# Optimization experiments

Hardware: AMD Instinct MI355X
Metric: run time of the kernel (lower is better)

The kernel has to match this reference:

```python
import jax, jax.numpy as jnp
import numpy as np

Q_HEADS, KV_HEADS, DIMS, IN_DIMS = 16, 4, 1024, 1024
HEAD_D = DIMS // Q_HEADS            # 64
GROUPS = Q_HEADS // KV_HEADS        # 4
ROPE_BASE = 10000.0


def nd_rope(x, coords):
    """N-D rotary embedding.
    x: [..., s, d]; coords: broadcastable [..., s, a] (float).
    Head dim d is split into a contiguous chunks of d//a; within each chunk
    consecutive pairs (2i, 2i+1) are rotated by angle coord_axis * base^(-2i/(d//a)).
    """
    a = coords.shape[-1]
    d = x.shape[-1]
    dpa = d // a                                  # dims per coordinate axis (even)
    inv_freq = ROPE_BASE ** (-jnp.arange(dpa // 2, dtype=jnp.float32) * (2.0 / dpa))
    angles = coords[..., :, None] * inv_freq      # [..., s, a, dpa//2]
    angles = angles.reshape(angles.shape[:-2] + (d // 2,))
    cos, sin = jnp.cos(angles), jnp.sin(angles)
    xp = x.reshape(x.shape[:-1] + (d // 2, 2))
    x1, x2 = xp[..., 0], xp[..., 1]
    return jnp.stack([x1 * cos - x2 * sin, x1 * sin + x2 * cos], axis=-1).reshape(x.shape)


def setup_inputs() -> dict:
    key = jax.random.key(0)
    k1, k2, k3, k4, k5, k6, k7, k8 = jax.random.split(key, 8)
    B, SQ, SKV, A = 4, 2048, 2048, 2
    q = jax.random.normal(k1, (B, SQ, IN_DIMS), dtype=jnp.float32)
    kv = jax.random.normal(k2, (B, SKV, IN_DIMS), dtype=jnp.float32)
    q_coords = jax.random.randint(k3, (B, SQ, A), 0, 2048, dtype=jnp.int32)
    kv_coords = jax.random.randint(k4, (B, SKV, A), 0, 2048, dtype=jnp.int32)
    s_in = 1.0 / np.sqrt(IN_DIMS)
    Wq = jax.random.normal(k5, (IN_DIMS, Q_HEADS, HEAD_D), dtype=jnp.float32) * s_in
    Wk = jax.random.normal(k6, (IN_DIMS, KV_HEADS, HEAD_D), dtype=jnp.float32) * s_in
    Wv = jax.random.normal(k7, (IN_DIMS, KV_HEADS, HEAD_D), dtype=jnp.float32) * s_in
    Wo = jax.random.normal(k8, (KV_HEADS * HEAD_D, IN_DIMS), dtype=jnp.float32) * (1.0 / np.sqrt(KV_HEADS * HEAD_D))
    return {"q": q, "q_coords": q_coords, "kv": kv, "kv_coords": kv_coords,
            "Wq": Wq, "Wk": Wk, "Wv": Wv, "Wo": Wo}


def reference(q, q_coords, kv, kv_coords, Wq, Wk, Wv, Wo):
    B, SQ = q.shape[0], q.shape[1]
    qp = jnp.einsum('bsi,ihd->bshd', q, Wq)   # [b, sq, q_heads, hd]
    kp = jnp.einsum('bsi,ihd->bshd', kv, Wk)  # [b, skv, kv_heads, hd]
    vp = jnp.einsum('bsi,ihd->bshd', kv, Wv)
    # '... s (h g) d -> ... g h s d' with h=KV_HEADS outer, g=GROUPS inner
    qp = qp.reshape(B, SQ, KV_HEADS, GROUPS, HEAD_D).transpose(0, 3, 2, 1, 4)  # [b,g,h,sq,hd]
    kp = kp.transpose(0, 2, 1, 3)  # [b,h,skv,hd]
    vp = vp.transpose(0, 2, 1, 3)
    qc = q_coords.astype(jnp.float32)[:, None, None]  # [b,1,1,sq,a] -> broadcast over g,h
    kc = kv_coords.astype(jnp.float32)[:, None]       # [b,1,skv,a] -> broadcast over h
    qr = nd_rope(qp, qc)
    kr = nd_rope(kp, kc)
    # NOTE: einops pattern omits g in output -> group axis is SUMMED (faithful to source)
    scores = jnp.einsum('bghsd,bhad->bhsa', qr, kr) / (HEAD_D ** 0.5)
    attn = jax.nn.softmax(scores, axis=-1)
    out = jnp.einsum('bhsa,bhad->bhsd', attn, vp)
    out = out.transpose(0, 2, 1, 3).reshape(B, SQ, KV_HEADS * HEAD_D)
    return out @ Wo
```

## Files before the change

kernel.cpp:

```cpp
#include <hip/hip_runtime.h>

#define BATCH 4
#define SEQQ  2048
#define SEQKV 2048
#define NH    4
#define HD    64
#define IND   1024
#define QSCL 0.18033688011112042f

typedef __attribute__((ext_vector_type(8))) short short8;
typedef __attribute__((ext_vector_type(4))) short s4v;
typedef __attribute__((ext_vector_type(4))) float floatx4;

#if defined(__HIP_DEVICE_COMPILE__) && __has_builtin(__builtin_amdgcn_exp2f)
  #define EXP2(x) __builtin_amdgcn_exp2f(x)
#else
  #define EXP2(x) exp2f(x)
#endif

#if defined(__HIP_DEVICE_COMPILE__)
  #if __has_builtin(__builtin_amdgcn_mfma_f32_16x16x16bf16_1k)
    #define MFMA16(a, b, c) __builtin_amdgcn_mfma_f32_16x16x16bf16_1k(a, b, c, 0, 0, 0)
  #elif __has_builtin(__builtin_amdgcn_mfma_f32_16x16x16_bf16)
    #define MFMA16(a, b, c) __builtin_amdgcn_mfma_f32_16x16x16_bf16(a, b, c, 0, 0, 0)
  #else
    #error "no 16x16x16 bf16 MFMA builtin on gfx950 device pass"
  #endif
#else
  #define MFMA16(a, b, c) (c)
#endif
#define MFMA32(a, b, c) __builtin_amdgcn_mfma_f32_16x16x32_bf16(a, b, c, 0, 0, 0)

__device__ __forceinline__ short f2b(float f) {
    unsigned u; __builtin_memcpy(&u, &f, 4);
    u = (u + 0x7fffu + ((u >> 16) & 1u)) >> 16;
    return (short)u;
}
__device__ __forceinline__ short8 cvt8(const float* p) {
    float4 a = *(const float4*)p;
    float4 b = *(const float4*)(p + 4);
    short8 r;
    r[0] = f2b(a.x); r[1] = f2b(a.y); r[2] = f2b(a.z); r[3] = f2b(a.w);
    r[4] = f2b(b.x); r[5] = f2b(b.y); r[6] = f2b(b.z); r[7] = f2b(b.w);
    return r;
}

__global__ __launch_bounds__(256) void prep_all(
    const float* __restrict__ Wq, const float* __restrict__ Wk,
    const float* __restrict__ Wv, const float* __restrict__ Wo,
    const float* __restrict__ q, const float* __restrict__ kv,
    short* __restrict__ Wq_t, short* __restrict__ Wkv_t, short* __restrict__ Wo_t,
    short* __restrict__ qb, short* __restrict__ kvb) {
    __shared__ short Ts[64][65];
    int blk = blockIdx.x;
    if (blk < 256) {
        int c4 = threadIdx.x & 63, r4 = threadIdx.x >> 6;
        if (blk < 64) {
            int h = blk & 3, ib = blk >> 2;
#pragma unroll 4
            for (int jj = 0; jj < 16; ++jj) {
                int il = r4 * 16 + jj;
                float s = 0.f;
#pragma unroll
                for (int g = 0; g < 4; ++g)
                    s += Wq[(ib * 64 + il) * 1024 + (h * 4 + g) * 64 + c4];
                Ts[il][c4] = f2b(s);
            }
            __syncthreads();
#pragma unroll 4
            for (int jj = 0; jj < 16; ++jj) {
                int dl = r4 * 16 + jj;
                Wq_t[(h * 64 + dl) * 1024 + ib * 64 + c4] = Ts[c4][dl];
            }
        } else if (blk < 192) {
            int t = blk - 64, ss = t >> 6; t &= 63;
            int ib = t >> 2, nb = t & 3;
            const float* W = ss ? Wv : Wk;
#pragma unroll 4
            for (int jj = 0; jj < 16; ++jj) {
                int il = r4 * 16 + jj;
                Ts[il][c4] = f2b(W[(ib * 64 + il) * 256 + nb * 64 + c4]);
            }
            __syncthreads();
#pragma unroll 4
            for (int jj = 0; jj < 16; ++jj) {
                int dl = r4 * 16 + jj;
                Wkv_t[(ss * 256 + nb * 64 + dl) * 1024 + ib * 64 + c4] = Ts[c4][dl];
            }
        } else {
            int t = blk - 192, kb = t >> 4, nb = t & 15;
#pragma unroll 4
            for (int jj = 0; jj < 16; ++jj) {
                int il = r4 * 16 + jj;
                Ts[il][c4] = f2b(Wo[(kb * 64 + il) * 1024 + nb * 64 + c4]);
            }
            __syncthreads();
#pragma unroll 4
            for (int jj = 0; jj < 16; ++jj) {
                int dl = r4 * 16 + jj;
                Wo_t[(nb * 64 + dl) * 256 + kb * 64 + c4] = Ts[c4][dl];
            }
        }
    } else if (blk < 2304) {
        long e = ((long)(blk - 256) * 256 + threadIdx.x) * 16;
        *(short8*)(qb + e)     = cvt8(q + e);
        *(short8*)(qb + e + 8) = cvt8(q + e + 8);
    } else {
        long e = ((long)(blk - 2304) * 256 + threadIdx.x) * 16;
        *(short8*)(kvb + e)     = cvt8(kv + e);
        *(short8*)(kvb + e + 8) = cvt8(kv + e + 8);
    }
}

template <int MODE>
__device__ __forceinline__ void gemm128(
    const short* __restrict__ A, const short* __restrict__ Wt,
    int m0, int n0, int N, int K, short* As, short* Bs,
    float* __restrict__ C, const int* __restrict__ coords,
    short* __restrict__ ropeDst, short* __restrict__ vDst) {
    const int t = threadIdx.x;
    const int w = t >> 6, lane = t & 63, ln = lane & 15, quad = lane >> 4;
    const int wm = w >> 1, wn = w & 1;
    const int srow = lane >> 2, skc = (lane & 3) * 8;
    floatx4 acc[4][4];
#pragma unroll
    for (int mt = 0; mt < 4; ++mt)
#pragma unroll
        for (int nt = 0; nt < 4; ++nt) acc[mt][nt] = floatx4{0.f, 0.f, 0.f, 0.f};

    for (int ks = 0; ks < K; ks += 32) {
        __syncthreads();
#pragma unroll
        for (int i = 0; i < 2; ++i) {
            __builtin_amdgcn_global_load_lds(
                (const void*)(A + (long)(m0 + w * 32 + i * 16 + srow) * K + ks + skc),
                (void*)(As + (w * 2 + i) * 512), 16, 0, 0);
            __builtin_amdgcn_global_load_lds(
                (const void*)(Wt + (long)(n0 + w * 32 + i * 16 + srow) * K + ks + skc),
                (void*)(Bs + (w * 2 + i) * 512), 16, 0, 0);
        }
        __syncthreads();
        short8 af[4], bf[4];
#pragma unroll
        for (int mt = 0; mt < 4; ++mt)
            af[mt] = *(const short8*)(As + (wm * 64 + mt * 16 + ln) * 32 + quad * 8);
#pragma unroll
        for (int nt = 0; nt < 4; ++nt)
            bf[nt] = *(const short8*)(Bs + (wn * 64 + nt * 16 + ln) * 32 + quad * 8);
#pragma unroll
        for (int mt = 0; mt < 4; ++mt)
#pragma unroll
            for (int nt = 0; nt < 4; ++nt)
                acc[mt][nt] = MFMA32(af[mt], bf[nt], acc[mt][nt]);
    }

    if (MODE == 0) {
#pragma unroll
        for (int mt = 0; mt < 4; ++mt) {
            int row0 = m0 + wm * 64 + mt * 16 + quad * 4;
#pragma unroll
            for (int nt = 0; nt < 4; ++nt) {
                int col = n0 + wn * 64 + nt * 16 + ln;
#pragma unroll
                for (int r = 0; r < 4; ++r)
                    C[(long)(row0 + r) * N + col] = acc[mt][nt][r];
            }
        }
    } else {
        const int wn_col = n0 + wn * 64;
        if (MODE == 1 || wn_col < 256) {
            const int h = (wn_col >> 6) & 3;
            const float scl = (MODE == 1) ? QSCL : 1.0f;
            const float L = -0.5756462732485114f;
            const float fA = __expf((float)(ln >> 1) * L);
            const float fB = __expf((float)(8 + (ln >> 1)) * L);
            const float sgn = (ln & 1) ? 1.0f : -1.0f;
#pragma unroll
            for (int mt = 0; mt < 4; ++mt) {
                int row0 = m0 + wm * 64 + mt * 16 + quad * 4;
#pragma unroll
                for (int r = 0; r < 4; ++r) {
                    int row = row0 + r;
                    float c0 = (float)coords[row * 2];
                    float c1 = (float)coords[row * 2 + 1];
                    float snv[4], csv[4];
                    __sincosf(c0 * fA, &snv[0], &csv[0]);
                    __sincosf(c0 * fB, &snv[1], &csv[1]);
                    __sincosf(c1 * fA, &snv[2], &csv[2]);
                    __sincosf(c1 * fB, &snv[3], &csv[3]);
                    long rbase = ((long)((row >> 11) * 4 + h) * 2048 + (row & 2047)) * 64;
#pragma unroll
                    for (int nt = 0; nt < 4; ++nt) {
                        float v = acc[mt][nt][r];
                        float p = __shfl_xor(v, 1, 64);
                        float o = v * (csv[nt] * scl) + p * (snv[nt] * (scl * sgn));
                        ropeDst[rbase + nt * 16 + ln] = f2b(o);
                    }
                }
            }
        } else {
            const int h = ((wn_col - 256) >> 6) & 3;
#pragma unroll
            for (int mt = 0; mt < 4; ++mt) {
                int row0 = m0 + wm * 64 + mt * 16 + quad * 4;
                int b = row0 >> 11, s0 = row0 & 2047;
#pragma unroll
                for (int nt = 0; nt < 4; ++nt) {
                    s4v ov;
#pragma unroll
                    for (int r = 0; r < 4; ++r) ov[r] = f2b(acc[mt][nt][r]);
                    *(s4v*)(vDst + (long)((b * 4 + h) * 64 + nt * 16 + ln) * 2048 + s0) = ov;
                }
            }
        }
    }
}

__global__ __launch_bounds__(256) void proj_gemm(
    const short* __restrict__ qb, const short* __restrict__ kvb,
    const short* __restrict__ Wq_t, const short* __restrict__ Wkv_t,
    const int* __restrict__ qc, const int* __restrict__ kvc,
    short* __restrict__ Qr, short* __restrict__ Kr, short* __restrict__ Vt) {
    __shared__ __align__(16) short As[128 * 32];
    __shared__ __align__(16) short Bs[128 * 32];
    int id = blockIdx.x;
    if (id < 128)
        gemm128<1>(qb, Wq_t, (id >> 1) * 128, (id & 1) * 128, 256, 1024, As, Bs,
                   nullptr, qc, Qr, nullptr);
    else {
        int t = id - 128;
        gemm128<2>(kvb, Wkv_t, (t >> 2) * 128, (t & 3) * 128, 512, 1024, As, Bs,
                   nullptr, kvc, Kr, Vt);
    }
}

__global__ __launch_bounds__(256) void final_gemm(
    const short* __restrict__ Ob, const short* __restrict__ Wo_t, float* __restrict__ out) {
    __shared__ __align__(16) short As[128 * 32];
    __shared__ __align__(16) short Bs[128 * 32];
    gemm128<0>(Ob, Wo_t, blockIdx.x * 128, blockIdx.y * 128, 1024, 256, As, Bs,
               out, nullptr, nullptr, nullptr);
}

__global__ __launch_bounds__(256, 4) void attn_kernel(
    const short* __restrict__ Qr, const short* __restrict__ Kr,
    const short* __restrict__ Vt, float* __restrict__ Op, float* __restrict__ Lp) {
    __shared__ __align__(16) short Kls[2][64 * 64];
    __shared__ __align__(16) short Vls[2][64 * 64];
    const int blk = blockIdx.x;
    const int bh = blk & 15, sp = (blk >> 4) & 3, qg = blk >> 6;
    const int w = threadIdx.x >> 6, lane = threadIdx.x & 63;
    const int ln = lane & 15, quad = lane >> 4;
    const int q0 = qg * 128 + w * 32;
    const short* Qb = Qr + (long)bh * SEQKV * HD;
    const short* Kb = Kr + (long)bh * SEQKV * HD;
    const short* Vb = Vt + (long)bh * HD * SEQKV;

    const int srow = lane >> 3;
    const int schk = (lane & 7) ^ (srow & 7);
    const long kstage0 = (long)(w * 16 + srow) * HD + schk * 8;
    const long vstage0 = (long)(w * 16 + srow) * SEQKV + schk * 8;

    short8 qf[2][2];
#pragma unroll
    for (int qs = 0; qs < 2; ++qs)
#pragma unroll
        for (int ck = 0; ck < 2; ++ck)
            qf[qs][ck] = *(const short8*)(Qb + (long)(q0 + qs * 16 + ln) * HD + ck * 32 + quad * 8);

    s4v ones;
#pragma unroll
    for (int j = 0; j < 4; ++j) ones[j] = (short)0x3F80;

    floatx4 o[2][4], ol[2];
#pragma unroll
    for (int qs = 0; qs < 2; ++qs) {
        ol[qs] = floatx4{0.f, 0.f, 0.f, 0.f};
#pragma unroll
        for (int nt = 0; nt < 4; ++nt) o[qs][nt] = floatx4{0.f, 0.f, 0.f, 0.f};
    }

    const int ln7 = ln & 7;
    int koff[2];
#pragma unroll
    for (int ck = 0; ck < 2; ++ck) koff[ck] = ln * 64 + ((ck * 4 + quad) ^ ln7) * 8;
    int voff[4];
#pragma unroll
    for (int t = 0; t < 4; ++t) voff[t] = ln * 64 + ((t * 2 + (quad >> 1)) ^ ln7) * 8 + (quad & 1) * 4;

    const int kt0 = sp * 512;
#define STAGE(kt, sel)                                                              \
    do {                                                                            \
        _Pragma("unroll")                                                           \
        for (int i = 0; i < 2; ++i) {                                               \
            __builtin_amdgcn_global_load_lds(                                       \
                (const void*)(Kb + (long)(kt) * HD + kstage0 + (long)i * 8 * HD),   \
                (void*)(Kls[sel] + (w * 16 + i * 8) * 64), 16, 0, 0);               \
            __builtin_amdgcn_global_load_lds(                                       \
                (const void*)(Vb + (kt) + vstage0 + (long)i * 8 * SEQKV),           \
                (void*)(Vls[sel] + (w * 16 + i * 8) * 64), 16, 0, 0);               \
        }                                                                           \
    } while (0)

    STAGE(kt0, 0);
    __syncthreads();
    int cur = 0;
    for (int tt = 0; tt < 8; ++tt) {
        if (tt < 7) STAGE(kt0 + (tt + 1) * 64, cur ^ 1);
        const short* Kc = Kls[cur];
        const short* Vc = Vls[cur];
#pragma unroll
        for (int t = 0; t < 4; ++t) {
            short8 a0 = *(const short8*)(Kc + t * 1024 + koff[0]);
            short8 a1 = *(const short8*)(Kc + t * 1024 + koff[1]);
            floatx4 st0 = {0.f, 0.f, 0.f, 0.f}, st1 = {0.f, 0.f, 0.f, 0.f};
            st0 = MFMA32(a0, qf[0][0], st0);
            st1 = MFMA32(a0, qf[1][0], st1);
            st0 = MFMA32(a1, qf[0][1], st0);
            st1 = MFMA32(a1, qf[1][1], st1);
            s4v pt0, pt1;
#pragma unroll
            for (int j = 0; j < 4; ++j) {
                float p0 = EXP2(st0[j]);
                float p1 = EXP2(st1[j]);
                unsigned u0, u1;
                __builtin_memcpy(&u0, &p0, 4); __builtin_memcpy(&u1, &p1, 4);
                pt0[j] = (short)((u0 + 0x8000u) >> 16);
                pt1[j] = (short)((u1 + 0x8000u) >> 16);
            }
#pragma unroll
            for (int nt = 0; nt < 4; ++nt) {
                s4v vf = *(const s4v*)(Vc + nt * 1024 + voff[t]);
                o[0][nt] = MFMA16(vf, pt0, o[0][nt]);
                o[1][nt] = MFMA16(vf, pt1, o[1][nt]);
            }
            ol[0] = MFMA16(ones, pt0, ol[0]);
            ol[1] = MFMA16(ones, pt1, ol[1]);
        }
        __syncthreads();
        cur ^= 1;
    }
#undef STAGE
#pragma unroll
    for (int qs = 0; qs < 2; ++qs) {
        long qrow = (long)(sp * 16 + bh) * 2048 + q0 + qs * 16 + ln;
        if (quad == 0) Lp[qrow] = ol[qs][0];
#pragma unroll
        for (int nt = 0; nt < 4; ++nt)
            *(floatx4*)(Op + qrow * 64 + nt * 16 + quad * 4) = o[qs][nt];
    }
}

__global__ __launch_bounds__(256) void combine_kernel(
    const float* __restrict__ Op, const float* __restrict__ Lp, short* __restrict__ Ob) {
    int idx = blockIdx.x * 256 + threadIdx.x;
    int row = idx >> 4;
    int d0 = (idx & 15) * 4;
    int bh = row >> 11, qq = row & 2047;
    int b = bh >> 2, h = bh & 3;
    float4 os = {0.f, 0.f, 0.f, 0.f};
    float ls = 0.f;
#pragma unroll
    for (int s = 0; s < 4; ++s) {
        long rr = (long)(s * 16 + bh) * 2048 + qq;
        float4 v = *(const float4*)(Op + rr * 64 + d0);
        os.x += v.x; os.y += v.y; os.z += v.z; os.w += v.w;
        ls += Lp[rr];
    }
    float li = 1.f / ls;
    s4v ov;
    ov[0] = f2b(os.x * li); ov[1] = f2b(os.y * li);
    ov[2] = f2b(os.z * li); ov[3] = f2b(os.w * li);
    *(s4v*)(Ob + ((long)(b * 2048 + qq)) * 256 + h * 64 + d0) = ov;
}

extern "C" void kernel_launch(void* const* d_in, const int* in_sizes, int n_in,
                              void* d_out, int out_size, void* d_ws, size_t ws_size,
                              hipStream_t stream) {
    const float* q   = (const float*)d_in[0];
    const int*   qc  = (const int*)d_in[1];
    const float* kv  = (const float*)d_in[2];
    const int*   kvc = (const int*)d_in[3];
    const float* Wq  = (const float*)d_in[4];
    const float* Wk  = (const float*)d_in[5];
    const float* Wv  = (const float*)d_in[6];
    const float* Wo  = (const float*)d_in[7];
    float* out = (float*)d_out;

    char* ws = (char*)d_ws;
    const size_t MB = 1024 * 1024;
    short* Wq_t  = (short*)(ws);
    short* Wkv_t = (short*)(ws + MB / 2);
    short* Wo_t  = (short*)(ws + 3 * MB / 2);
    short* qb    = (short*)(ws + 2 * MB);
    short* kvb   = (short*)(ws + 18 * MB);
    short* Qr    = (short*)(ws + 34 * MB);
    short* Kr    = (short*)(ws + 38 * MB);
    short* Vt    = (short*)(ws + 42 * MB);
    short* Ob    = (short*)(ws + 46 * MB);
    float* Opart = (float*)(ws + 50 * MB);
    float* Lpart = (float*)(ws + 82 * MB);

    hipLaunchKernelGGL(prep_all, dim3(4352), dim3(256), 0, stream,
                       Wq, Wk, Wv, Wo, q, kv, Wq_t, Wkv_t, Wo_t, qb, kvb);
    hipLaunchKernelGGL(proj_gemm, dim3(384), dim3(256), 0, stream,
                       qb, kvb, Wq_t, Wkv_t, qc, kvc, Qr, Kr, Vt);
    hipLaunchKernelGGL(attn_kernel, dim3(1024), dim3(256), 0, stream,
                       Qr, Kr, Vt, Opart, Lpart);
    hipLaunchKernelGGL(combine_kernel, dim3(2048), dim3(256), 0, stream,
                       Opart, Lpart, Ob);
    hipLaunchKernelGGL(final_gemm, dim3(64, 8), dim3(256), 0, stream, Ob, Wo_t, out);
}
```

Baseline: 191.3 us.

## Double-buffer GEMM LDS staging and use packed bf16 convert with setprio in attention

The shared GEMM routine now keeps two LDS buffers, so the next K-slice is loaded while MFMAs run on the current one, and each iteration needs one barrier instead of two. The attention inner loop replaces the manual round-to-bf16 bit manipulation with the hardware v_cvt_pk_bf16_f32 instruction. It also wraps the MFMA groups in s_setprio so waves issuing matrix work get priority. Doubling LDS per GEMM block may lower occupancy. The hardware convert's rounding may differ slightly from the old round-half-up code.

```diff
diff --git a/kernel.cpp b/kernel.cpp
--- a/kernel.cpp
+++ b/kernel.cpp
@@ -128,30 +128,40 @@
 #pragma unroll
         for (int nt = 0; nt < 4; ++nt) acc[mt][nt] = floatx4{0.f, 0.f, 0.f, 0.f};
 
-    for (int ks = 0; ks < K; ks += 32) {
-        __syncthreads();
+    auto stage = [&](int ks, int sel) {
 #pragma unroll
         for (int i = 0; i < 2; ++i) {
             __builtin_amdgcn_global_load_lds(
                 (const void*)(A + (long)(m0 + w * 32 + i * 16 + srow) * K + ks + skc),
-                (void*)(As + (w * 2 + i) * 512), 16, 0, 0);
+                (void*)(As + sel * 4096 + (w * 2 + i) * 512), 16, 0, 0);
             __builtin_amdgcn_global_load_lds(
                 (const void*)(Wt + (long)(n0 + w * 32 + i * 16 + srow) * K + ks + skc),
-                (void*)(Bs + (w * 2 + i) * 512), 16, 0, 0);
+                (void*)(Bs + sel * 4096 + (w * 2 + i) * 512), 16, 0, 0);
         }
-        __syncthreads();
+    };
+
+    const int nk = K >> 5;
+    stage(0, 0);
+    __syncthreads();
+    int cur = 0;
+    for (int tt = 0; tt < nk; ++tt) {
+        if (tt < nk - 1) stage((tt + 1) * 32, cur ^ 1);
+        const short* Ac = As + cur * 4096;
+        const short* Bc = Bs + cur * 4096;
         short8 af[4], bf[4];
 #pragma unroll
         for (int mt = 0; mt < 4; ++mt)
-            af[mt] = *(const short8*)(As + (wm * 64 + mt * 16 + ln) * 32 + quad * 8);
+            af[mt] = *(const short8*)(Ac + (wm * 64 + mt * 16 + ln) * 32 + quad * 8);
 #pragma unroll
         for (int nt = 0; nt < 4; ++nt)
-            bf[nt] = *(const short8*)(Bs + (wn * 64 + nt * 16 + ln) * 32 + quad * 8);
+            bf[nt] = *(const short8*)(Bc + (wn * 64 + nt * 16 + ln) * 32 + quad * 8);
 #pragma unroll
         for (int mt = 0; mt < 4; ++mt)
 #pragma unroll
             for (int nt = 0; nt < 4; ++nt)
                 acc[mt][nt] = MFMA32(af[mt], bf[nt], acc[mt][nt]);
+        __syncthreads();
+        cur ^= 1;
     }
 
     if (MODE == 0) {
@@ -221,25 +231,25 @@
     const short* __restrict__ Wq_t, const short* __restrict__ Wkv_t,
     const int* __restrict__ qc, const int* __restrict__ kvc,
     short* __restrict__ Qr, short* __restrict__ Kr, short* __restrict__ Vt) {
-    __shared__ __align__(16) short As[128 * 32];
-    __shared__ __align__(16) short Bs[128 * 32];
+    __shared__ __align__(16) short As[2][128 * 32];
+    __shared__ __align__(16) short Bs[2][128 * 32];
     int id = blockIdx.x;
     if (id < 128)
-        gemm128<1>(qb, Wq_t, (id >> 1) * 128, (id & 1) * 128, 256, 1024, As, Bs,
-                   nullptr, qc, Qr, nullptr);
+        gemm128<1>(qb, Wq_t, (id >> 1) * 128, (id & 1) * 128, 256, 1024,
+                   &As[0][0], &Bs[0][0], nullptr, qc, Qr, nullptr);
     else {
         int t = id - 128;
-        gemm128<2>(kvb, Wkv_t, (t >> 2) * 128, (t & 3) * 128, 512, 1024, As, Bs,
-                   nullptr, kvc, Kr, Vt);
+        gemm128<2>(kvb, Wkv_t, (t >> 2) * 128, (t & 3) * 128, 512, 1024,
+                   &As[0][0], &Bs[0][0], nullptr, kvc, Kr, Vt);
     }
 }
 
 __global__ __launch_bounds__(256) void final_gemm(
     const short* __restrict__ Ob, const short* __restrict__ Wo_t, float* __restrict__ out) {
-    __shared__ __align__(16) short As[128 * 32];
-    __shared__ __align__(16) short Bs[128 * 32];
-    gemm128<0>(Ob, Wo_t, blockIdx.x * 128, blockIdx.y * 128, 1024, 256, As, Bs,
-               out, nullptr, nullptr, nullptr);
+    __shared__ __align__(16) short As[2][128 * 32];
+    __shared__ __align__(16) short Bs[2][128 * 32];
+    gemm128<0>(Ob, Wo_t, blockIdx.x * 128, blockIdx.y * 128, 1024, 256,
+               &As[0][0], &Bs[0][0], out, nullptr, nullptr, nullptr);
 }
 
 __global__ __launch_bounds__(256, 4) void attn_kernel(
@@ -314,20 +324,23 @@
             short8 a0 = *(const short8*)(Kc + t * 1024 + koff[0]);
             short8 a1 = *(const short8*)(Kc + t * 1024 + koff[1]);
             floatx4 st0 = {0.f, 0.f, 0.f, 0.f}, st1 = {0.f, 0.f, 0.f, 0.f};
+            __builtin_amdgcn_s_setprio(1);
             st0 = MFMA32(a0, qf[0][0], st0);
             st1 = MFMA32(a0, qf[1][0], st1);
             st0 = MFMA32(a1, qf[0][1], st0);
             st1 = MFMA32(a1, qf[1][1], st1);
+            __builtin_amdgcn_s_setprio(0);
+            float e0 = EXP2(st0[0]), e1 = EXP2(st0[1]), e2 = EXP2(st0[2]), e3 = EXP2(st0[3]);
+            float g0 = EXP2(st1[0]), g1 = EXP2(st1[1]), g2 = EXP2(st1[2]), g3 = EXP2(st1[3]);
+            unsigned a0p, a1p, b0p, b1p;
+            asm("v_cvt_pk_bf16_f32 %0, %1, %2" : "=v"(a0p) : "v"(e0), "v"(e1));
+            asm("v_cvt_pk_bf16_f32 %0, %1, %2" : "=v"(a1p) : "v"(e2), "v"(e3));
+            asm("v_cvt_pk_bf16_f32 %0, %1, %2" : "=v"(b0p) : "v"(g0), "v"(g1));
+            asm("v_cvt_pk_bf16_f32 %0, %1, %2" : "=v"(b1p) : "v"(g2), "v"(g3));
             s4v pt0, pt1;
-#pragma unroll
-            for (int j = 0; j < 4; ++j) {
-                float p0 = EXP2(st0[j]);
-                float p1 = EXP2(st1[j]);
-                unsigned u0, u1;
-                __builtin_memcpy(&u0, &p0, 4); __builtin_memcpy(&u1, &p1, 4);
-                pt0[j] = (short)((u0 + 0x8000u) >> 16);
-                pt1[j] = (short)((u1 + 0x8000u) >> 16);
-            }
+            { unsigned tmp[2] = {a0p, a1p}; __builtin_memcpy(&pt0, tmp, 8); }
+            { unsigned tmp[2] = {b0p, b1p}; __builtin_memcpy(&pt1, tmp, 8); }
+            __builtin_amdgcn_s_setprio(1);
 #pragma unroll
             for (int nt = 0; nt < 4; ++nt) {
                 s4v vf = *(const s4v*)(Vc + nt * 1024 + voff[t]);
@@ -336,6 +349,7 @@
             }
             ol[0] = MFMA16(ones, pt0, ol[0]);
             ol[1] = MFMA16(ones, pt1, ol[1]);
+            __builtin_amdgcn_s_setprio(0);
         }
         __syncthreads();
         cur ^= 1;
```

Measured after the change: 193.6 us. About the same (+1.2%).
